# Optimization experiments

Measured on AMD Instinct MI355X. Metric: run time of the kernel, lower is better.

The kernel has to match this reference:

```python
import jax, jax.numpy as jnp
import numpy as np

EPS = 1e-10

def _retrieve(q, kv, norm):
    # q: [b,h,n,d], kv: [b,h,d,e], norm: [b,h,d]
    numer = jnp.einsum('bhnd,bhde->bhne', q, kv)
    denom = jnp.einsum('bhnd,bhd->bhn', q, norm)
    return numer / jnp.clip(denom, EPS)[..., None]

def setup_inputs() -> dict:
    key = jax.random.key(0)
    ks = jax.random.split(key, 6)
    B, H, N, D, E = 4, 16, 8192, 64, 64
    return {
        'keys': jax.random.normal(ks[0], (B, H, N, D), jnp.float32),
        'values': jax.random.normal(ks[1], (B, H, N, E), jnp.float32),
        'queries': jax.random.normal(ks[2], (B, H, N, D), jnp.float32),
        'out': jax.random.normal(ks[3], (B, H, N, E), jnp.float32),
        'past_kv': jax.random.normal(ks[4], (B, H, D, E), jnp.float32),
        'past_norm': jax.random.uniform(ks[5], (B, H, D), jnp.float32) + 0.5,
        'head_gates': jnp.ones((H,), jnp.float32) * 10.0,
    }

def reference(keys, values, queries, out, past_kv, past_norm, head_gates):
    # create_new_memories (with delta rule)
    k = jax.nn.elu(keys) + 1.0
    delta_v = _retrieve(k, past_kv, past_norm)
    v = values - delta_v
    new_kv = jnp.einsum('bhnd,bhne->bhde', k, v) + past_kv
    new_norm = k.sum(axis=-2) + past_norm
    # retrieve_and_add_to_output (reads past memories)
    q = jax.nn.elu(queries) + 1.0
    mem_out = _retrieve(q, past_kv, past_norm)
    gates = jax.nn.sigmoid(head_gates)[:, None, None]  # [h,1,1]
    out_g = out * gates + mem_out * (1.0 - gates)
    return out_g, new_kv, new_norm
```

## Files before the change

kernel.cpp:

```cpp
#include <hip/hip_runtime.h>

constexpr int BH   = 64;
constexpr int NN   = 8192;
constexpr int DD   = 64;
constexpr int EE   = 64;
constexpr int ST   = 72;
constexpr int NSPLIT = 32;
constexpr int ROWS = NN / NSPLIT;
constexpr int CHUNK = 64;
constexpr float EPS_ = 1e-10f;

typedef __attribute__((ext_vector_type(8))) short short8;
typedef __attribute__((ext_vector_type(4))) float f32x4;

#define MFMA16(a, b, c) __builtin_amdgcn_mfma_f32_16x16x32_bf16((a), (b), (c), 0, 0, 0)

__device__ __forceinline__ unsigned short f2bf(float f) {
  union { float f; unsigned u; } v; v.f = f;
  unsigned r = v.u + 0x7fffu + ((v.u >> 16) & 1u);
  return (unsigned short)(r >> 16);
}
__device__ __forceinline__ float bf2f(unsigned short s) {
  union { unsigned u; float f; } v; v.u = ((unsigned)s) << 16;
  return v.f;
}
__device__ __forceinline__ float elu1(float x) {
  return x > 0.0f ? x + 1.0f : __expf(x);
}

__global__ void fw_init_kernel(const float* __restrict__ past_kv,
                               const float* __restrict__ past_norm,
                               float* __restrict__ out_kv,
                               float* __restrict__ out_norm) {
  int i = blockIdx.x * 256 + threadIdx.x;
  if (i < BH * DD * EE) out_kv[i] = past_kv[i];
  if (i < BH * DD)      out_norm[i] = past_norm[i];
}

__global__ __launch_bounds__(256, 3) void fw_kv_kernel(
    const float* __restrict__ keys, const float* __restrict__ values,
    const float* __restrict__ past_kv, const float* __restrict__ past_norm,
    float* __restrict__ out_kv, float* __restrict__ out_norm) {
  __shared__ unsigned short pkvT[EE * ST];
  __shared__ unsigned short kls [CHUNK * ST];
  __shared__ unsigned short kT  [DD * ST];
  __shared__ unsigned short vls [CHUNK * ST];
  __shared__ unsigned short vT  [EE * ST];
  __shared__ float pnorm_s[DD];
  __shared__ float denom_s[CHUNK];
  __shared__ float norm_part[DD];

  const int t  = threadIdx.x;
  const int bh = blockIdx.x & (BH - 1);
  const int split = blockIdx.x >> 6;
  const int row0 = split * ROWS;
  const long kvbase = (long)bh * NN * DD;

  if (t < DD) { pnorm_s[t] = past_norm[bh * DD + t]; norm_part[t] = 0.0f; }
  for (int p = 0; p < 4; ++p) {
    int idx = p * 1024 + t * 4;
    int d = idx >> 6, e0 = idx & 63;
    float4 v4 = *(const float4*)&past_kv[(long)bh * DD * EE + idx];
    pkvT[(e0 + 0) * ST + d] = f2bf(v4.x);
    pkvT[(e0 + 1) * ST + d] = f2bf(v4.y);
    pkvT[(e0 + 2) * ST + d] = f2bf(v4.z);
    pkvT[(e0 + 3) * ST + d] = f2bf(v4.w);
  }
  __syncthreads();

  const int l = t & 63, w = t >> 6;
  const int l16 = l & 15, q = l >> 4;

  float na0 = 0.f, na1 = 0.f, na2 = 0.f, na3 = 0.f;
  f32x4 acc2[4];
  #pragma unroll
  for (int i = 0; i < 4; ++i) acc2[i] = (f32x4){0.f, 0.f, 0.f, 0.f};

  for (int c = 0; c < ROWS / CHUNK; ++c) {
    const int rowc = row0 + c * CHUNK;

    for (int p = 0; p < 4; ++p) {
      int idx = p * 1024 + t * 4;
      int nl = idx >> 6;
      int d0 = idx & 63;
      float4 k4 = *(const float4*)&keys[kvbase + (long)(rowc + nl) * DD + d0];
      float k0 = elu1(k4.x), k1 = elu1(k4.y), k2 = elu1(k4.z), k3 = elu1(k4.w);
      ushort4 kb; kb.x = f2bf(k0); kb.y = f2bf(k1); kb.z = f2bf(k2); kb.w = f2bf(k3);
      *(ushort4*)&kls[nl * ST + d0] = kb;
      kT[(d0 + 0) * ST + nl] = kb.x;
      kT[(d0 + 1) * ST + nl] = kb.y;
      kT[(d0 + 2) * ST + nl] = kb.z;
      kT[(d0 + 3) * ST + nl] = kb.w;
      float part = k0 * pnorm_s[d0] + k1 * pnorm_s[d0 + 1]
                 + k2 * pnorm_s[d0 + 2] + k3 * pnorm_s[d0 + 3];
      part += __shfl_xor(part, 1);
      part += __shfl_xor(part, 2);
      part += __shfl_xor(part, 4);
      part += __shfl_xor(part, 8);
      if (l16 == 0) denom_s[nl] = part;
      na0 += k0; na1 += k1; na2 += k2; na3 += k3;
      float4 v4 = *(const float4*)&values[kvbase + (long)(rowc + nl) * DD + d0];
      ushort4 vb; vb.x = f2bf(v4.x); vb.y = f2bf(v4.y); vb.z = f2bf(v4.z); vb.w = f2bf(v4.w);
      *(ushort4*)&vls[nl * ST + d0] = vb;
    }
    __syncthreads();

    const int nb = w * 16;
    f32x4 acc1[4];
    #pragma unroll
    for (int i = 0; i < 4; ++i) acc1[i] = (f32x4){0.f, 0.f, 0.f, 0.f};
    #pragma unroll
    for (int s = 0; s < 2; ++s) {
      short8 bfrag = *(const short8*)&kls[(nb + l16) * ST + s * 32 + q * 8];
      #pragma unroll
      for (int et = 0; et < 4; ++et) {
        short8 afrag = *(const short8*)&pkvT[(et * 16 + l16) * ST + s * 32 + q * 8];
        acc1[et] = MFMA16(afrag, bfrag, acc1[et]);
      }
    }
    const float rd = 1.0f / fmaxf(denom_s[nb + l16], EPS_);
    #pragma unroll
    for (int et = 0; et < 4; ++et) {
      #pragma unroll
      for (int i = 0; i < 4; ++i) {
        int e = et * 16 + q * 4 + i;
        float val = bf2f(vls[(nb + l16) * ST + e]);
        float v = val - acc1[et][i] * rd;
        vT[e * ST + nb + l16] = f2bf(v);
      }
    }
    __syncthreads();

    #pragma unroll
    for (int s = 0; s < 2; ++s) {
      short8 afrag = *(const short8*)&vT[(w * 16 + l16) * ST + s * 32 + q * 8];
      #pragma unroll
      for (int dt = 0; dt < 4; ++dt) {
        short8 bfrag = *(const short8*)&kT[(dt * 16 + l16) * ST + s * 32 + q * 8];
        acc2[dt] = MFMA16(afrag, bfrag, acc2[dt]);
      }
    }
    __syncthreads();
  }

  {
    const int d0 = (t & 15) * 4;
    atomicAdd(&norm_part[d0 + 0], na0);
    atomicAdd(&norm_part[d0 + 1], na1);
    atomicAdd(&norm_part[d0 + 2], na2);
    atomicAdd(&norm_part[d0 + 3], na3);
  }
  __syncthreads();
  if (t < DD) atomicAdd(&out_norm[bh * DD + t], norm_part[t]);
  #pragma unroll
  for (int dt = 0; dt < 4; ++dt) {
    #pragma unroll
    for (int i = 0; i < 4; ++i) {
      int d = dt * 16 + l16;
      int e = w * 16 + q * 4 + i;
      atomicAdd(&out_kv[(long)bh * DD * EE + d * EE + e], acc2[dt][i]);
    }
  }
}

__global__ __launch_bounds__(256, 4) void fw_out_kernel(
    const float* __restrict__ queries, const float* __restrict__ outin,
    const float* __restrict__ past_kv, const float* __restrict__ past_norm,
    const float* __restrict__ head_gates, float* __restrict__ out_g) {
  __shared__ unsigned short pkvT[EE * ST];
  __shared__ unsigned short qls [CHUNK * ST];
  __shared__ unsigned short mem_s[CHUNK * ST];
  __shared__ float pnorm_s[DD];
  __shared__ float denom_s[CHUNK];

  const int t  = threadIdx.x;
  const int bh = blockIdx.x & (BH - 1);
  const int split = blockIdx.x >> 6;
  const int row0 = split * ROWS;
  const long qbase = (long)bh * NN * DD;

  const float hg = head_gates[bh & 15];
  const float g = 1.0f / (1.0f + __expf(-hg));
  const float gm1 = 1.0f - g;

  if (t < DD) pnorm_s[t] = past_norm[bh * DD + t];
  for (int p = 0; p < 4; ++p) {
    int idx = p * 1024 + t * 4;
    int d = idx >> 6, e0 = idx & 63;
    float4 v4 = *(const float4*)&past_kv[(long)bh * DD * EE + idx];
    pkvT[(e0 + 0) * ST + d] = f2bf(v4.x);
    pkvT[(e0 + 1) * ST + d] = f2bf(v4.y);
    pkvT[(e0 + 2) * ST + d] = f2bf(v4.z);
    pkvT[(e0 + 3) * ST + d] = f2bf(v4.w);
  }
  __syncthreads();

  const int l = t & 63, w = t >> 6;
  const int l16 = l & 15, q = l >> 4;

  for (int c = 0; c < ROWS / CHUNK; ++c) {
    const int rowc = row0 + c * CHUNK;

    for (int p = 0; p < 4; ++p) {
      int idx = p * 1024 + t * 4;
      int nl = idx >> 6, d0 = idx & 63;
      float4 q4 = *(const float4*)&queries[qbase + (long)(rowc + nl) * DD + d0];
      float q0 = elu1(q4.x), q1 = elu1(q4.y), q2 = elu1(q4.z), q3 = elu1(q4.w);
      ushort4 qb; qb.x = f2bf(q0); qb.y = f2bf(q1); qb.z = f2bf(q2); qb.w = f2bf(q3);
      *(ushort4*)&qls[nl * ST + d0] = qb;
      float part = q0 * pnorm_s[d0] + q1 * pnorm_s[d0 + 1]
                 + q2 * pnorm_s[d0 + 2] + q3 * pnorm_s[d0 + 3];
      part += __shfl_xor(part, 1);
      part += __shfl_xor(part, 2);
      part += __shfl_xor(part, 4);
      part += __shfl_xor(part, 8);
      if (l16 == 0) denom_s[nl] = part;
    }
    __syncthreads();

    const int nb = w * 16;
    f32x4 acc[4];
    #pragma unroll
    for (int i = 0; i < 4; ++i) acc[i] = (f32x4){0.f, 0.f, 0.f, 0.f};
    #pragma unroll
    for (int s = 0; s < 2; ++s) {
      short8 bfrag = *(const short8*)&qls[(nb + l16) * ST + s * 32 + q * 8];
      #pragma unroll
      for (int et = 0; et < 4; ++et) {
        short8 afrag = *(const short8*)&pkvT[(et * 16 + l16) * ST + s * 32 + q * 8];
        acc[et] = MFMA16(afrag, bfrag, acc[et]);
      }
    }
    const float rd = 1.0f / fmaxf(denom_s[nb + l16], EPS_);
    #pragma unroll
    for (int et = 0; et < 4; ++et) {
      #pragma unroll
      for (int i = 0; i < 4; ++i) {
        int e = et * 16 + q * 4 + i;
        mem_s[(nb + l16) * ST + e] = f2bf(acc[et][i] * rd);
      }
    }
    __syncthreads();

    for (int p = 0; p < 4; ++p) {
      int idx = p * 1024 + t * 4;
      int nl = idx >> 6, e0 = idx & 63;
      ushort4 mb = *(const ushort4*)&mem_s[nl * ST + e0];
      long goff = qbase + (long)(rowc + nl) * EE + e0;
      float4 o4 = *(const float4*)&outin[goff];
      float4 r;
      r.x = o4.x * g + bf2f(mb.x) * gm1;
      r.y = o4.y * g + bf2f(mb.y) * gm1;
      r.z = o4.z * g + bf2f(mb.z) * gm1;
      r.w = o4.w * g + bf2f(mb.w) * gm1;
      *(float4*)&out_g[goff] = r;
    }
  }
}

extern "C" void kernel_launch(void* const* d_in, const int* in_sizes, int n_in,
                              void* d_out, int out_size, void* d_ws, size_t ws_size,
                              hipStream_t stream) {
  const float* keys      = (const float*)d_in[0];
  const float* values    = (const float*)d_in[1];
  const float* queries   = (const float*)d_in[2];
  const float* outin     = (const float*)d_in[3];
  const float* past_kv   = (const float*)d_in[4];
  const float* past_norm = (const float*)d_in[5];
  const float* head_gates= (const float*)d_in[6];

  float* out_g    = (float*)d_out;
  float* out_kv   = out_g + (long)BH * NN * EE;
  float* out_norm = out_kv + (long)BH * DD * EE;

  fw_init_kernel<<<(BH * DD * EE + 255) / 256, 256, 0, stream>>>(
      past_kv, past_norm, out_kv, out_norm);
  fw_kv_kernel<<<BH * NSPLIT, 256, 0, stream>>>(
      keys, values, past_kv, past_norm, out_kv, out_norm);
  fw_out_kernel<<<BH * NSPLIT, 256, 0, stream>>>(
      queries, outin, past_kv, past_norm, head_gates, out_g);
}
```

Measured before the change: 583.4 us.

## Merge kv and output kernels into one interleaved launch with register prefetch

Fuses the kv-update and output-retrieval kernels into a single launch. Block indices are interleaved so that one in three blocks handles a kv split and two handle output splits, letting the two workloads run side by side on the GPU. Each chunk's keys/values or queries/out rows are prefetched into registers while the current chunk is processed, overlapping global loads with MFMA work. The kv path reads values directly into registers in fragment layout and drops the values LDS buffer. This raises register pressure and halves the number of kv splits, which gives longer per-block kv loops.

Result: faster. 550.7 us (-5.6%).

```diff
diff --git a/kernel.cpp b/kernel.cpp
--- a/kernel.cpp
+++ b/kernel.cpp
@@ -5,9 +5,13 @@
 constexpr int DD   = 64;
 constexpr int EE   = 64;
 constexpr int ST   = 72;
-constexpr int NSPLIT = 32;
-constexpr int ROWS = NN / NSPLIT;
+constexpr int NSPLIT_KV  = 16;
+constexpr int NSPLIT_OUT = 32;
+constexpr int ROWS_KV  = NN / NSPLIT_KV;
+constexpr int ROWS_OUT = NN / NSPLIT_OUT;
 constexpr int CHUNK = 64;
+constexpr int NCH_KV  = ROWS_KV / CHUNK;
+constexpr int NCH_OUT = ROWS_OUT / CHUNK;
 constexpr float EPS_ = 1e-10f;
 
 typedef __attribute__((ext_vector_type(8))) short short8;
@@ -37,223 +41,233 @@
   if (i < BH * DD)      out_norm[i] = past_norm[i];
 }
 
-__global__ __launch_bounds__(256, 3) void fw_kv_kernel(
+__global__ __launch_bounds__(256, 4) void fw_main_kernel(
     const float* __restrict__ keys, const float* __restrict__ values,
+    const float* __restrict__ queries, const float* __restrict__ outin,
     const float* __restrict__ past_kv, const float* __restrict__ past_norm,
+    const float* __restrict__ head_gates, float* __restrict__ out_g,
     float* __restrict__ out_kv, float* __restrict__ out_norm) {
   __shared__ unsigned short pkvT[EE * ST];
-  __shared__ unsigned short kls [CHUNK * ST];
+  __shared__ unsigned short bufN[CHUNK * ST];
   __shared__ unsigned short kT  [DD * ST];
-  __shared__ unsigned short vls [CHUNK * ST];
-  __shared__ unsigned short vT  [EE * ST];
+  __shared__ unsigned short bufE[EE * ST];
   __shared__ float pnorm_s[DD];
   __shared__ float denom_s[CHUNK];
   __shared__ float norm_part[DD];
 
-  const int t  = threadIdx.x;
-  const int bh = blockIdx.x & (BH - 1);
-  const int split = blockIdx.x >> 6;
-  const int row0 = split * ROWS;
-  const long kvbase = (long)bh * NN * DD;
+  const int t   = threadIdx.x;
+  const int bid = blockIdx.x;
+  const int rem = bid % 3;
+  const int sub = bid / 3;
+
+  int bh, row0;
+  if (rem == 0) {
+    bh = sub & (BH - 1); row0 = (sub >> 6) * ROWS_KV;
+  } else {
+    int oidx = sub * 2 + rem - 1;
+    bh = oidx & (BH - 1); row0 = (oidx >> 6) * ROWS_OUT;
+  }
 
   if (t < DD) { pnorm_s[t] = past_norm[bh * DD + t]; norm_part[t] = 0.0f; }
+  #pragma unroll
   for (int p = 0; p < 4; ++p) {
     int idx = p * 1024 + t * 4;
     int d = idx >> 6, e0 = idx & 63;
-    float4 v4 = *(const float4*)&past_kv[(long)bh * DD * EE + idx];
-    pkvT[(e0 + 0) * ST + d] = f2bf(v4.x);
-    pkvT[(e0 + 1) * ST + d] = f2bf(v4.y);
-    pkvT[(e0 + 2) * ST + d] = f2bf(v4.z);
-    pkvT[(e0 + 3) * ST + d] = f2bf(v4.w);
+    f32x4 v4 = *(const f32x4*)&past_kv[(long)bh * DD * EE + idx];
+    pkvT[(e0 + 0) * ST + d] = f2bf(v4[0]);
+    pkvT[(e0 + 1) * ST + d] = f2bf(v4[1]);
+    pkvT[(e0 + 2) * ST + d] = f2bf(v4[2]);
+    pkvT[(e0 + 3) * ST + d] = f2bf(v4[3]);
   }
   __syncthreads();
 
   const int l = t & 63, w = t >> 6;
   const int l16 = l & 15, q = l >> 4;
-
-  float na0 = 0.f, na1 = 0.f, na2 = 0.f, na3 = 0.f;
-  f32x4 acc2[4];
-  #pragma unroll
-  for (int i = 0; i < 4; ++i) acc2[i] = (f32x4){0.f, 0.f, 0.f, 0.f};
-
-  for (int c = 0; c < ROWS / CHUNK; ++c) {
-    const int rowc = row0 + c * CHUNK;
-
+  const int d0 = (t & 15) * 4;
+  const int r0 = t >> 4;
+  const int nb = w * 16;
+  const long gbase = (long)bh * NN * DD;
+
+  if (rem == 0) {
+    f32x4 kreg[4], vreg[4];
+    #pragma unroll
     for (int p = 0; p < 4; ++p) {
-      int idx = p * 1024 + t * 4;
-      int nl = idx >> 6;
-      int d0 = idx & 63;
-      float4 k4 = *(const float4*)&keys[kvbase + (long)(rowc + nl) * DD + d0];
-      float k0 = elu1(k4.x), k1 = elu1(k4.y), k2 = elu1(k4.z), k3 = elu1(k4.w);
-      ushort4 kb; kb.x = f2bf(k0); kb.y = f2bf(k1); kb.z = f2bf(k2); kb.w = f2bf(k3);
-      *(ushort4*)&kls[nl * ST + d0] = kb;
-      kT[(d0 + 0) * ST + nl] = kb.x;
-      kT[(d0 + 1) * ST + nl] = kb.y;
-      kT[(d0 + 2) * ST + nl] = kb.z;
-      kT[(d0 + 3) * ST + nl] = kb.w;
-      float part = k0 * pnorm_s[d0] + k1 * pnorm_s[d0 + 1]
-                 + k2 * pnorm_s[d0 + 2] + k3 * pnorm_s[d0 + 3];
-      part += __shfl_xor(part, 1);
-      part += __shfl_xor(part, 2);
-      part += __shfl_xor(part, 4);
-      part += __shfl_xor(part, 8);
-      if (l16 == 0) denom_s[nl] = part;
-      na0 += k0; na1 += k1; na2 += k2; na3 += k3;
-      float4 v4 = *(const float4*)&values[kvbase + (long)(rowc + nl) * DD + d0];
-      ushort4 vb; vb.x = f2bf(v4.x); vb.y = f2bf(v4.y); vb.z = f2bf(v4.z); vb.w = f2bf(v4.w);
-      *(ushort4*)&vls[nl * ST + d0] = vb;
-    }
-    __syncthreads();
-
-    const int nb = w * 16;
-    f32x4 acc1[4];
-    #pragma unroll
-    for (int i = 0; i < 4; ++i) acc1[i] = (f32x4){0.f, 0.f, 0.f, 0.f};
-    #pragma unroll
-    for (int s = 0; s < 2; ++s) {
-      short8 bfrag = *(const short8*)&kls[(nb + l16) * ST + s * 32 + q * 8];
+      kreg[p] = *(const f32x4*)&keys[gbase + (long)(row0 + p * 16 + r0) * DD + d0];
+      vreg[p] = *(const f32x4*)&values[gbase + (long)(row0 + nb + l16) * EE + p * 16 + q * 4];
+    }
+    float na0 = 0.f, na1 = 0.f, na2 = 0.f, na3 = 0.f;
+    f32x4 acc2[4];
+    #pragma unroll
+    for (int i = 0; i < 4; ++i) acc2[i] = (f32x4){0.f, 0.f, 0.f, 0.f};
+
+    for (int c = 0; c < NCH_KV; ++c) {
+      #pragma unroll
+      for (int p = 0; p < 4; ++p) {
+        const int nl = p * 16 + r0;
+        float k0 = elu1(kreg[p][0]), k1 = elu1(kreg[p][1]);
+        float k2 = elu1(kreg[p][2]), k3 = elu1(kreg[p][3]);
+        ushort4 kb; kb.x = f2bf(k0); kb.y = f2bf(k1); kb.z = f2bf(k2); kb.w = f2bf(k3);
+        *(ushort4*)&bufN[nl * ST + d0] = kb;
+        kT[(d0 + 0) * ST + nl] = kb.x;
+        kT[(d0 + 1) * ST + nl] = kb.y;
+        kT[(d0 + 2) * ST + nl] = kb.z;
+        kT[(d0 + 3) * ST + nl] = kb.w;
+        float part = k0 * pnorm_s[d0] + k1 * pnorm_s[d0 + 1]
+                   + k2 * pnorm_s[d0 + 2] + k3 * pnorm_s[d0 + 3];
+        part += __shfl_xor(part, 1);
+        part += __shfl_xor(part, 2);
+        part += __shfl_xor(part, 4);
+        part += __shfl_xor(part, 8);
+        if (l16 == 0) denom_s[nl] = part;
+        na0 += k0; na1 += k1; na2 += k2; na3 += k3;
+      }
+      const bool more = (c + 1 < NCH_KV);
+      f32x4 kregN[4], vregN[4];
+      if (more) {
+        const int rown = row0 + (c + 1) * CHUNK;
+        #pragma unroll
+        for (int p = 0; p < 4; ++p) {
+          kregN[p] = *(const f32x4*)&keys[gbase + (long)(rown + p * 16 + r0) * DD + d0];
+          vregN[p] = *(const f32x4*)&values[gbase + (long)(rown + nb + l16) * EE + p * 16 + q * 4];
+        }
+      }
+      __syncthreads();
+
+      f32x4 acc1[4];
+      #pragma unroll
+      for (int i = 0; i < 4; ++i) acc1[i] = (f32x4){0.f, 0.f, 0.f, 0.f};
+      #pragma unroll
+      for (int s = 0; s < 2; ++s) {
+        short8 bfrag = *(const short8*)&bufN[(nb + l16) * ST + s * 32 + q * 8];
+        #pragma unroll
+        for (int et = 0; et < 4; ++et) {
+          short8 afrag = *(const short8*)&pkvT[(et * 16 + l16) * ST + s * 32 + q * 8];
+          acc1[et] = MFMA16(afrag, bfrag, acc1[et]);
+        }
+      }
+      const float rd = 1.0f / fmaxf(denom_s[nb + l16], EPS_);
       #pragma unroll
       for (int et = 0; et < 4; ++et) {
-        short8 afrag = *(const short8*)&pkvT[(et * 16 + l16) * ST + s * 32 + q * 8];
-        acc1[et] = MFMA16(afrag, bfrag, acc1[et]);
-      }
-    }
-    const float rd = 1.0f / fmaxf(denom_s[nb + l16], EPS_);
-    #pragma unroll
-    for (int et = 0; et < 4; ++et) {
-      #pragma unroll
-      for (int i = 0; i < 4; ++i) {
-        int e = et * 16 + q * 4 + i;
-        float val = bf2f(vls[(nb + l16) * ST + e]);
-        float v = val - acc1[et][i] * rd;
-        vT[e * ST + nb + l16] = f2bf(v);
-      }
-    }
-    __syncthreads();
-
-    #pragma unroll
-    for (int s = 0; s < 2; ++s) {
-      short8 afrag = *(const short8*)&vT[(w * 16 + l16) * ST + s * 32 + q * 8];
-      #pragma unroll
-      for (int dt = 0; dt < 4; ++dt) {
-        short8 bfrag = *(const short8*)&kT[(dt * 16 + l16) * ST + s * 32 + q * 8];
-        acc2[dt] = MFMA16(afrag, bfrag, acc2[dt]);
-      }
-    }
-    __syncthreads();
-  }
-
-  {
-    const int d0 = (t & 15) * 4;
+        #pragma unroll
+        for (int i = 0; i < 4; ++i) {
+          const int e = et * 16 + q * 4 + i;
+          bufE[e * ST + nb + l16] = f2bf(vreg[et][i] - acc1[et][i] * rd);
+        }
+      }
+      __syncthreads();
+
+      #pragma unroll
+      for (int s = 0; s < 2; ++s) {
+        short8 afrag = *(const short8*)&bufE[(nb + l16) * ST + s * 32 + q * 8];
+        #pragma unroll
+        for (int dt = 0; dt < 4; ++dt) {
+          short8 bfrag = *(const short8*)&kT[(dt * 16 + l16) * ST + s * 32 + q * 8];
+          acc2[dt] = MFMA16(afrag, bfrag, acc2[dt]);
+        }
+      }
+      __syncthreads();
+
+      if (more) {
+        #pragma unroll
+        for (int p = 0; p < 4; ++p) { kreg[p] = kregN[p]; vreg[p] = vregN[p]; }
+      }
+    }
+
     atomicAdd(&norm_part[d0 + 0], na0);
     atomicAdd(&norm_part[d0 + 1], na1);
     atomicAdd(&norm_part[d0 + 2], na2);
     atomicAdd(&norm_part[d0 + 3], na3);
-  }
-  __syncthreads();
-  if (t < DD) atomicAdd(&out_norm[bh * DD + t], norm_part[t]);
-  #pragma unroll
-  for (int dt = 0; dt < 4; ++dt) {
-    #pragma unroll
-    for (int i = 0; i < 4; ++i) {
-      int d = dt * 16 + l16;
-      int e = w * 16 + q * 4 + i;
-      atomicAdd(&out_kv[(long)bh * DD * EE + d * EE + e], acc2[dt][i]);
-    }
-  }
-}
-
-__global__ __launch_bounds__(256, 4) void fw_out_kernel(
-    const float* __restrict__ queries, const float* __restrict__ outin,
-    const float* __restrict__ past_kv, const float* __restrict__ past_norm,
-    const float* __restrict__ head_gates, float* __restrict__ out_g) {
-  __shared__ unsigned short pkvT[EE * ST];
-  __shared__ unsigned short qls [CHUNK * ST];
-  __shared__ unsigned short mem_s[CHUNK * ST];
-  __shared__ float pnorm_s[DD];
-  __shared__ float denom_s[CHUNK];
-
-  const int t  = threadIdx.x;
-  const int bh = blockIdx.x & (BH - 1);
-  const int split = blockIdx.x >> 6;
-  const int row0 = split * ROWS;
-  const long qbase = (long)bh * NN * DD;
-
-  const float hg = head_gates[bh & 15];
-  const float g = 1.0f / (1.0f + __expf(-hg));
-  const float gm1 = 1.0f - g;
-
-  if (t < DD) pnorm_s[t] = past_norm[bh * DD + t];
-  for (int p = 0; p < 4; ++p) {
-    int idx = p * 1024 + t * 4;
-    int d = idx >> 6, e0 = idx & 63;
-    float4 v4 = *(const float4*)&past_kv[(long)bh * DD * EE + idx];
-    pkvT[(e0 + 0) * ST + d] = f2bf(v4.x);
-    pkvT[(e0 + 1) * ST + d] = f2bf(v4.y);
-    pkvT[(e0 + 2) * ST + d] = f2bf(v4.z);
-    pkvT[(e0 + 3) * ST + d] = f2bf(v4.w);
-  }
-  __syncthreads();
-
-  const int l = t & 63, w = t >> 6;
-  const int l16 = l & 15, q = l >> 4;
-
-  for (int c = 0; c < ROWS / CHUNK; ++c) {
-    const int rowc = row0 + c * CHUNK;
-
+    __syncthreads();
+    if (t < DD) atomicAdd(&out_norm[bh * DD + t], norm_part[t]);
+    #pragma unroll
+    for (int dt = 0; dt < 4; ++dt) {
+      #pragma unroll
+      for (int i = 0; i < 4; ++i) {
+        const int d = dt * 16 + l16;
+        const int e = nb + q * 4 + i;
+        atomicAdd(&out_kv[(long)bh * DD * EE + d * EE + e], acc2[dt][i]);
+      }
+    }
+  } else {
+    const float hg = head_gates[bh & 15];
+    const float g = 1.0f / (1.0f + __expf(-hg));
+    const float gm1 = 1.0f - g;
+
+    f32x4 qreg[4], oreg[4];
+    #pragma unroll
     for (int p = 0; p < 4; ++p) {
-      int idx = p * 1024 + t * 4;
-      int nl = idx >> 6, d0 = idx & 63;
-      float4 q4 = *(const float4*)&queries[qbase + (long)(rowc + nl) * DD + d0];
-      float q0 = elu1(q4.x), q1 = elu1(q4.y), q2 = elu1(q4.z), q3 = elu1(q4.w);
-      ushort4 qb; qb.x = f2bf(q0); qb.y = f2bf(q1); qb.z = f2bf(q2); qb.w = f2bf(q3);
-      *(ushort4*)&qls[nl * ST + d0] = qb;
-      float part = q0 * pnorm_s[d0] + q1 * pnorm_s[d0 + 1]
-                 + q2 * pnorm_s[d0 + 2] + q3 * pnorm_s[d0 + 3];
-      part += __shfl_xor(part, 1);
-      part += __shfl_xor(part, 2);
-      part += __shfl_xor(part, 4);
-      part += __shfl_xor(part, 8);
-      if (l16 == 0) denom_s[nl] = part;
-    }
-    __syncthreads();
-
-    const int nb = w * 16;
-    f32x4 acc[4];
-    #pragma unroll
-    for (int i = 0; i < 4; ++i) acc[i] = (f32x4){0.f, 0.f, 0.f, 0.f};
-    #pragma unroll
-    for (int s = 0; s < 2; ++s) {
-      short8 bfrag = *(const short8*)&qls[(nb + l16) * ST + s * 32 + q * 8];
+      qreg[p] = *(const f32x4*)&queries[gbase + (long)(row0 + p * 16 + r0) * DD + d0];
+      oreg[p] = *(const f32x4*)&outin[gbase + (long)(row0 + p * 16 + r0) * EE + d0];
+    }
+
+    for (int c = 0; c < NCH_OUT; ++c) {
+      const int rowc = row0 + c * CHUNK;
+      #pragma unroll
+      for (int p = 0; p < 4; ++p) {
+        const int nl = p * 16 + r0;
+        float q0 = elu1(qreg[p][0]), q1 = elu1(qreg[p][1]);
+        float q2 = elu1(qreg[p][2]), q3 = elu1(qreg[p][3]);
+        ushort4 qb; qb.x = f2bf(q0); qb.y = f2bf(q1); qb.z = f2bf(q2); qb.w = f2bf(q3);
+        *(ushort4*)&bufN[nl * ST + d0] = qb;
+        float part = q0 * pnorm_s[d0] + q1 * pnorm_s[d0 + 1]
+                   + q2 * pnorm_s[d0 + 2] + q3 * pnorm_s[d0 + 3];
+        part += __shfl_xor(part, 1);
+        part += __shfl_xor(part, 2);
+        part += __shfl_xor(part, 4);
+        part += __shfl_xor(part, 8);
+        if (l16 == 0) denom_s[nl] = part;
+      }
+      const bool more = (c + 1 < NCH_OUT);
+      f32x4 qregN[4], oregN[4];
+      if (more) {
+        const int rown = rowc + CHUNK;
+        #pragma unroll
+        for (int p = 0; p < 4; ++p) {
+          qregN[p] = *(const f32x4*)&queries[gbase + (long)(rown + p * 16 + r0) * DD + d0];
+          oregN[p] = *(const f32x4*)&outin[gbase + (long)(rown + p * 16 + r0) * EE + d0];
+        }
+      }
+      __syncthreads();
+
+      f32x4 acc[4];
+      #pragma unroll
+      for (int i = 0; i < 4; ++i) acc[i] = (f32x4){0.f, 0.f, 0.f, 0.f};
+      #pragma unroll
+      for (int s = 0; s < 2; ++s) {
+        short8 bfrag = *(const short8*)&bufN[(nb + l16) * ST + s * 32 + q * 8];
+        #pragma unroll
+        for (int et = 0; et < 4; ++et) {
+          short8 afrag = *(const short8*)&pkvT[(et * 16 + l16) * ST + s * 32 + q * 8];
+          acc[et] = MFMA16(afrag, bfrag, acc[et]);
+        }
+      }
+      const float rd = 1.0f / fmaxf(denom_s[nb + l16], EPS_);
       #pragma unroll
       for (int et = 0; et < 4; ++et) {
-        short8 afrag = *(const short8*)&pkvT[(et * 16 + l16) * ST + s * 32 + q * 8];
-        acc[et] = MFMA16(afrag, bfrag, acc[et]);
-      }
-    }
-    const float rd = 1.0f / fmaxf(denom_s[nb + l16], EPS_);
-    #pragma unroll
-    for (int et = 0; et < 4; ++et) {
-      #pragma unroll
-      for (int i = 0; i < 4; ++i) {
-        int e = et * 16 + q * 4 + i;
-        mem_s[(nb + l16) * ST + e] = f2bf(acc[et][i] * rd);
-      }
-    }
-    __syncthreads();
-
-    for (int p = 0; p < 4; ++p) {
-      int idx = p * 1024 + t * 4;
-      int nl = idx >> 6, e0 = idx & 63;
-      ushort4 mb = *(const ushort4*)&mem_s[nl * ST + e0];
-      long goff = qbase + (long)(rowc + nl) * EE + e0;
-      float4 o4 = *(const float4*)&outin[goff];
-      float4 r;
-      r.x = o4.x * g + bf2f(mb.x) * gm1;
-      r.y = o4.y * g + bf2f(mb.y) * gm1;
-      r.z = o4.z * g + bf2f(mb.z) * gm1;
-      r.w = o4.w * g + bf2f(mb.w) * gm1;
-      *(float4*)&out_g[goff] = r;
+        #pragma unroll
+        for (int i = 0; i < 4; ++i) {
+          const int e = et * 16 + q * 4 + i;
+          bufE[(nb + l16) * ST + e] = f2bf(acc[et][i] * rd);
+        }
+      }
+      __syncthreads();
+
+      #pragma unroll
+      for (int p = 0; p < 4; ++p) {
+        const int nl = p * 16 + r0;
+        ushort4 mb = *(const ushort4*)&bufE[nl * ST + d0];
+        f32x4 o = oreg[p];
+        f32x4 r;
+        r[0] = o[0] * g + bf2f(mb.x) * gm1;
+        r[1] = o[1] * g + bf2f(mb.y) * gm1;
+        r[2] = o[2] * g + bf2f(mb.z) * gm1;
+        r[3] = o[3] * g + bf2f(mb.w) * gm1;
+        *(f32x4*)&out_g[gbase + (long)(rowc + nl) * EE + d0] = r;
+      }
+      if (more) {
+        #pragma unroll
+        for (int p = 0; p < 4; ++p) { qreg[p] = qregN[p]; oreg[p] = oregN[p]; }
+      }
     }
   }
 }
@@ -275,8 +289,7 @@
 
   fw_init_kernel<<<(BH * DD * EE + 255) / 256, 256, 0, stream>>>(
       past_kv, past_norm, out_kv, out_norm);
-  fw_kv_kernel<<<BH * NSPLIT, 256, 0, stream>>>(
-      keys, values, past_kv, past_norm, out_kv, out_norm);
-  fw_out_kernel<<<BH * NSPLIT, 256, 0, stream>>>(
-      queries, outin, past_kv, past_norm, head_gates, out_g);
-}
+  fw_main_kernel<<<3 * BH * NSPLIT_KV, 256, 0, stream>>>(
+      keys, values, queries, outin, past_kv, past_norm, head_gates,
+      out_g, out_kv, out_norm);
+}
```
